# Performance work log

Measured on AMD Instinct MI355X. Metric: run time of the kernel, lower is better.

## Reference

```python
import jax, jax.numpy as jnp
import numpy as np

N = 128 * 128          # hardcoded in the original forward: x.view(1, 1, 128*128)
SCORE_LIMIT = int(0.5 * N)   # int(score_limit * num_inputs) = 8192
K = 7                  # odd kernel_size, padding = K // 2 = 3


def setup_inputs() -> dict:
    key = jax.random.key(0)
    k1, k2 = jax.random.split(key)
    x = jax.random.normal(k1, (N,), dtype=jnp.float32)
    # Conv1d(1, 1, K, bias=False) weight, flattened to a length-K taps vector
    conv_w = jax.random.normal(k2, (K,), dtype=jnp.float32) * 0.1
    return {"x": x, "conv_w": conv_w}


def reference(x, conv_w):
    # torch Conv1d is cross-correlation with 'same' padding (K odd):
    # y[i] = sum_j w[j] * x[i + j - K//2]. jnp.convolve flips the kernel,
    # so pass conv_w reversed to get cross-correlation.
    y = jnp.convolve(x, conv_w[::-1], mode="same")
    attention_score = jax.nn.sigmoid(y)                     # [N]
    attention_index = jnp.argsort(attention_score)          # ascending, [N]
    keep = attention_index[:SCORE_LIMIT]                    # lowest-score indices kept (as in source)
    simple_score = attention_score[keep] + 1.0              # [SCORE_LIMIT]
    # zeros everywhere, scatter rescaled values at kept indices
    new_x = jnp.zeros_like(x).at[keep].set(x[keep] * simple_score)
    return new_x, attention_score
```

## Files before the change

### kernel.cpp

```cpp
#include <hip/hip_runtime.h>
#include <math.h>

#define N 16384
#define LIMIT 8192
#define NT 1024
#define EPT 16

__global__ __launch_bounds__(1024) void fused_kernel(const float* __restrict__ x,
                                                     const float* __restrict__ w,
                                                     float* __restrict__ out) {
    __shared__ unsigned int hist[2048];
    __shared__ unsigned int partial[256];
    __shared__ unsigned long long prefix_sh;
    __shared__ unsigned int r_sh;

    const int tid = threadIdx.x;
    const int base = tid * EPT;

    float wv[7];
#pragma unroll
    for (int t = 0; t < 7; ++t) wv[t] = w[t];

    float win[EPT + 6];
    const float4* xv = (const float4*)(x + base);
#pragma unroll
    for (int q = 0; q < 4; ++q) {
        float4 v = xv[q];
        win[3 + 4*q + 0] = v.x; win[3 + 4*q + 1] = v.y;
        win[3 + 4*q + 2] = v.z; win[3 + 4*q + 3] = v.w;
    }
#pragma unroll
    for (int t = 0; t < 3; ++t) {
        int jl = base - 3 + t;
        win[t] = (jl >= 0) ? x[jl] : 0.f;
        int jr = base + EPT + t;
        win[EPT + 3 + t] = (jr < N) ? x[jr] : 0.f;
    }

    float s[EPT];
#pragma unroll
    for (int k = 0; k < EPT; ++k) {
        float acc = 0.f;
#pragma unroll
        for (int t = 0; t < 7; ++t)
            acc = __fadd_rn(acc, __fmul_rn(win[k + t], wv[t]));
        s[k] = 1.f / (1.f + expf(-acc));
    }

    float4* so = (float4*)(out + N + base);
#pragma unroll
    for (int q = 0; q < 4; ++q)
        so[q] = make_float4(s[4*q], s[4*q+1], s[4*q+2], s[4*q+3]);

    if (tid == 0) { prefix_sh = 0ULL; r_sh = LIMIT - 1; }

    for (int pass = 0; pass < 4; ++pass) {
        const int shift = 33 - 11 * pass;
        hist[tid] = 0u; hist[tid + 1024] = 0u;
        __syncthreads();
        const unsigned long long prefix = prefix_sh;
        const unsigned int r = r_sh;
#pragma unroll
        for (int k = 0; k < EPT; ++k) {
            unsigned long long key = ((unsigned long long)__float_as_uint(s[k]) << 14)
                                     | (unsigned int)(base + k);
            if ((key >> (shift + 11)) == prefix)
                atomicAdd(&hist[(unsigned int)(key >> shift) & 2047u], 1u);
        }
        __syncthreads();
        if (tid < 256) {
            unsigned int p = 0;
#pragma unroll
            for (int k = 0; k < 8; ++k) p += hist[tid * 8 + k];
            partial[tid] = p;
        }
        __syncthreads();
        if (tid < 64) {
            unsigned int p0 = partial[4*tid+0], p1 = partial[4*tid+1],
                         p2 = partial[4*tid+2], p3 = partial[4*tid+3];
            const unsigned int g = p0 + p1 + p2 + p3;
            unsigned int incl = g;
#pragma unroll
            for (int d = 1; d < 64; d <<= 1) {
                unsigned int up = __shfl_up(incl, d, 64);
                if (tid >= d) incl += up;
            }
            unsigned long long ball = __ballot(incl > r);
            int L = __ffsll((unsigned long long)ball) - 1;
            if (tid == L) {
                unsigned int cum = incl - g;
                unsigned int pp[4] = {p0, p1, p2, p3};
                int grp = -1;
#pragma unroll
                for (int k2 = 0; k2 < 4; ++k2) {
                    if (grp < 0) {
                        if (cum + pp[k2] > r) grp = 4*L + k2;
                        else cum += pp[k2];
                    }
                }
                unsigned int c[8];
#pragma unroll
                for (int k2 = 0; k2 < 8; ++k2) c[k2] = hist[grp*8 + k2];
                int b = -1;
#pragma unroll
                for (int k2 = 0; k2 < 8; ++k2) {
                    if (b < 0) {
                        if (cum + c[k2] > r) b = grp*8 + k2;
                        else cum += c[k2];
                    }
                }
                r_sh = r - cum;
                prefix_sh = (prefix << 11) | (unsigned long long)b;
            }
        }
        __syncthreads();
    }
    const unsigned long long T = prefix_sh;

    float4* no = (float4*)(out + base);
#pragma unroll
    for (int q = 0; q < 4; ++q) {
        float4 v;
        float* vp = &v.x;
#pragma unroll
        for (int e = 0; e < 4; ++e) {
            int k = 4*q + e;
            unsigned long long key = ((unsigned long long)__float_as_uint(s[k]) << 14)
                                     | (unsigned int)(base + k);
            vp[e] = (key <= T) ? __fmul_rn(win[3 + k], __fadd_rn(s[k], 1.0f)) : 0.f;
        }
        no[q] = v;
    }
}

extern "C" void kernel_launch(void* const* d_in, const int* in_sizes, int n_in,
                              void* d_out, int out_size, void* d_ws, size_t ws_size,
                              hipStream_t stream) {
    const float* x = (const float*)d_in[0];
    const float* w = (const float*)d_in[1];
    float* out = (float*)d_out;
    fused_kernel<<<1, NT, 0, stream>>>(x, w, out);
}
```

Baseline: 70.51 us.

## Split radix select across 16 cooperative blocks with compacted candidate keys

Moves the work from a single 1024-thread block to 16 cooperative blocks, one element per thread. A first 10-bit histogram pass is reduced across blocks in global memory, separated by grid syncs. Only keys that fall in the selected bucket are compacted into a workspace buffer, and the remaining radix passes run on those candidates alone. This is meant to remove the serial per-thread loop over 16 elements and the four full histogram passes in one block. It adds two grid-wide syncs, global atomics and workspace traffic, and every block redundantly repeats the candidate select.

```diff
diff --git a/kernel.cpp b/kernel.cpp
--- a/kernel.cpp
+++ b/kernel.cpp
@@ -1,136 +1,185 @@
 #include <hip/hip_runtime.h>
+#include <hip/hip_cooperative_groups.h>
 #include <math.h>
+
+namespace cg = cooperative_groups;
 
 #define N 16384
 #define LIMIT 8192
 #define NT 1024
-#define EPT 16
+#define G 16
 
-__global__ __launch_bounds__(1024) void fused_kernel(const float* __restrict__ x,
-                                                     const float* __restrict__ w,
-                                                     float* __restrict__ out) {
-    __shared__ unsigned int hist[2048];
-    __shared__ unsigned int partial[256];
+
+template <int W, int WIDTH>
+__device__ __forceinline__ void scan_select(unsigned int* tot,
+                                            unsigned int* partial,
+                                            unsigned long long* prefix_sh,
+                                            unsigned int* r_sh) {
+    const int tid = threadIdx.x;
+    const unsigned int r = *r_sh;
+    if (tid < 256) {
+        unsigned int p = 0;
+#pragma unroll
+        for (int q = 0; q < W / 4; ++q) {
+            uint4 v = ((const uint4*)tot)[tid * (W / 4) + q];
+            p += v.x + v.y + v.z + v.w;
+        }
+        partial[tid] = p;
+    }
+    __syncthreads();
+    if (tid < 64) {
+        unsigned int p0 = partial[4*tid+0], p1 = partial[4*tid+1],
+                     p2 = partial[4*tid+2], p3 = partial[4*tid+3];
+        const unsigned int g4 = p0 + p1 + p2 + p3;
+        unsigned int incl = g4;
+#pragma unroll
+        for (int d = 1; d < 64; d <<= 1) {
+            unsigned int up = __shfl_up(incl, d, 64);
+            if (tid >= d) incl += up;
+        }
+        unsigned long long ball = __ballot(incl > r);
+        int L = __ffsll((long long)ball) - 1;
+        if (tid == L) {
+            unsigned int cum = incl - g4;
+            unsigned int pp[4] = {p0, p1, p2, p3};
+            int grp = -1;
+#pragma unroll
+            for (int k = 0; k < 4; ++k)
+                if (grp < 0) { if (cum + pp[k] > r) grp = 4*L + k; else cum += pp[k]; }
+            unsigned int c[W];
+#pragma unroll
+            for (int q = 0; q < W / 4; ++q) {
+                uint4 v = ((const uint4*)tot)[grp * (W / 4) + q];
+                c[4*q+0] = v.x; c[4*q+1] = v.y; c[4*q+2] = v.z; c[4*q+3] = v.w;
+            }
+            int b = -1;
+#pragma unroll
+            for (int k = 0; k < W; ++k)
+                if (b < 0) { if (cum + c[k] > r) b = grp * W + k; else cum += c[k]; }
+            *r_sh = r - cum;
+            *prefix_sh = (*prefix_sh << WIDTH) | (unsigned long long)b;
+        }
+    }
+    __syncthreads();
+}
+
+__global__ __launch_bounds__(NT)
+void fused_kernel(const float* __restrict__ x, const float* __restrict__ w,
+                  float* __restrict__ out, unsigned int* __restrict__ ws) {
+    __shared__ __attribute__((aligned(16))) float lds_x[NT + 6];
+    __shared__ __attribute__((aligned(16))) unsigned int hist[4096];
+    __shared__ __attribute__((aligned(16))) unsigned int partial[256];
     __shared__ unsigned long long prefix_sh;
     __shared__ unsigned int r_sh;
 
     const int tid = threadIdx.x;
-    const int base = tid * EPT;
+    const int blk = blockIdx.x;
+    const int base = blk * NT;
+    const int i = base + tid;
+
+    unsigned int* gcnt = ws;
+    unsigned long long* keys = (unsigned long long*)(ws + 16);
+    unsigned int* ghist = ws + 16 + 2 * 16384;
+
+    if (blk == 0 && tid == 0) *gcnt = 0u;
 
     float wv[7];
 #pragma unroll
     for (int t = 0; t < 7; ++t) wv[t] = w[t];
 
-    float win[EPT + 6];
-    const float4* xv = (const float4*)(x + base);
+    lds_x[3 + tid] = x[i];
+    if (tid < 3) {
+        int jl = base - 3 + tid;
+        lds_x[tid] = (jl >= 0) ? x[jl] : 0.f;
+        int jr = base + NT + tid;
+        lds_x[NT + 3 + tid] = (jr < N) ? x[jr] : 0.f;
+    }
+    hist[tid] = 0u;
+    if (tid == 0) { prefix_sh = 0ULL; r_sh = LIMIT - 1; }
+    __syncthreads();
+
+    float acc = 0.f;
 #pragma unroll
-    for (int q = 0; q < 4; ++q) {
-        float4 v = xv[q];
-        win[3 + 4*q + 0] = v.x; win[3 + 4*q + 1] = v.y;
-        win[3 + 4*q + 2] = v.z; win[3 + 4*q + 3] = v.w;
+    for (int t = 0; t < 7; ++t)
+        acc = __fadd_rn(acc, __fmul_rn(lds_x[tid + t], wv[t]));
+    const float s = 1.f / (1.f + expf(-acc));
+    const float xi = lds_x[3 + tid];
+    out[N + i] = s;
+
+    const unsigned long long key =
+        ((unsigned long long)__float_as_uint(s) << 14) | (unsigned int)i;
+
+    atomicAdd(&hist[(unsigned int)(key >> 34)], 1u);
+    __syncthreads();
+    ghist[blk * NT + tid] = hist[tid];
+
+    __threadfence();
+    cg::this_grid().sync();
+
+    unsigned int tsum = 0;
+#pragma unroll
+    for (int b = 0; b < G; ++b) tsum += ghist[b * NT + tid];
+    hist[tid] = tsum;
+    __syncthreads();
+    scan_select<4, 10>(hist, partial, &prefix_sh, &r_sh);
+    const unsigned int b0 = (unsigned int)prefix_sh;
+    const unsigned int r0 = r_sh;
+
+    const bool cand = ((unsigned int)(key >> 34) == b0);
+    const unsigned long long m = __ballot(cand);
+    unsigned int wbase = 0;
+    if ((tid & 63) == 0 && m) wbase = atomicAdd(gcnt, (unsigned int)__popcll(m));
+    wbase = __shfl(wbase, 0, 64);
+    if (cand) {
+        unsigned int pos = wbase +
+            (unsigned int)__popcll(m & ((1ULL << (tid & 63)) - 1ULL));
+        keys[pos] = key;
     }
-#pragma unroll
-    for (int t = 0; t < 3; ++t) {
-        int jl = base - 3 + t;
-        win[t] = (jl >= 0) ? x[jl] : 0.f;
-        int jr = base + EPT + t;
-        win[EPT + 3 + t] = (jr < N) ? x[jr] : 0.f;
+    if (tid == 0) { prefix_sh = 0ULL; r_sh = r0; }
+    __threadfence();
+    cg::this_grid().sync();
+
+    const unsigned int C = __hip_atomic_load(gcnt, __ATOMIC_RELAXED,
+                                             __HIP_MEMORY_SCOPE_AGENT);
+
+    hist[tid] = 0; hist[tid+1024] = 0; hist[tid+2048] = 0; hist[tid+3072] = 0;
+    __syncthreads();
+    for (int j = tid; j < (int)C; j += NT) {
+        unsigned long long k34 = keys[j] & ((1ULL << 34) - 1ULL);
+        atomicAdd(&hist[(unsigned int)(k34 >> 22)], 1u);
     }
+    __syncthreads();
+    scan_select<16, 12>(hist, partial, &prefix_sh, &r_sh);
 
-    float s[EPT];
-#pragma unroll
-    for (int k = 0; k < EPT; ++k) {
-        float acc = 0.f;
-#pragma unroll
-        for (int t = 0; t < 7; ++t)
-            acc = __fadd_rn(acc, __fmul_rn(win[k + t], wv[t]));
-        s[k] = 1.f / (1.f + expf(-acc));
+    hist[tid] = 0; hist[tid+1024] = 0;
+    __syncthreads();
+    {
+        const unsigned long long pref = prefix_sh;
+        for (int j = tid; j < (int)C; j += NT) {
+            unsigned long long k34 = keys[j] & ((1ULL << 34) - 1ULL);
+            if ((k34 >> 22) == pref)
+                atomicAdd(&hist[(unsigned int)(k34 >> 11) & 2047u], 1u);
+        }
     }
+    __syncthreads();
+    scan_select<8, 11>(hist, partial, &prefix_sh, &r_sh);
 
-    float4* so = (float4*)(out + N + base);
-#pragma unroll
-    for (int q = 0; q < 4; ++q)
-        so[q] = make_float4(s[4*q], s[4*q+1], s[4*q+2], s[4*q+3]);
+    hist[tid] = 0; hist[tid+1024] = 0;
+    __syncthreads();
+    {
+        const unsigned long long pref = prefix_sh;
+        for (int j = tid; j < (int)C; j += NT) {
+            unsigned long long k34 = keys[j] & ((1ULL << 34) - 1ULL);
+            if ((k34 >> 11) == pref)
+                atomicAdd(&hist[(unsigned int)k34 & 2047u], 1u);
+        }
+    }
+    __syncthreads();
+    scan_select<8, 11>(hist, partial, &prefix_sh, &r_sh);
 
-    if (tid == 0) { prefix_sh = 0ULL; r_sh = LIMIT - 1; }
+    const unsigned long long T = ((unsigned long long)b0 << 34) | prefix_sh;
 
-    for (int pass = 0; pass < 4; ++pass) {
-        const int shift = 33 - 11 * pass;
-        hist[tid] = 0u; hist[tid + 1024] = 0u;
-        __syncthreads();
-        const unsigned long long prefix = prefix_sh;
-        const unsigned int r = r_sh;
-#pragma unroll
-        for (int k = 0; k < EPT; ++k) {
-            unsigned long long key = ((unsigned long long)__float_as_uint(s[k]) << 14)
-                                     | (unsigned int)(base + k);
-            if ((key >> (shift + 11)) == prefix)
-                atomicAdd(&hist[(unsigned int)(key >> shift) & 2047u], 1u);
-        }
-        __syncthreads();
-        if (tid < 256) {
-            unsigned int p = 0;
-#pragma unroll
-            for (int k = 0; k < 8; ++k) p += hist[tid * 8 + k];
-            partial[tid] = p;
-        }
-        __syncthreads();
-        if (tid < 64) {
-            unsigned int p0 = partial[4*tid+0], p1 = partial[4*tid+1],
-                         p2 = partial[4*tid+2], p3 = partial[4*tid+3];
-            const unsigned int g = p0 + p1 + p2 + p3;
-            unsigned int incl = g;
-#pragma unroll
-            for (int d = 1; d < 64; d <<= 1) {
-                unsigned int up = __shfl_up(incl, d, 64);
-                if (tid >= d) incl += up;
-            }
-            unsigned long long ball = __ballot(incl > r);
-            int L = __ffsll((unsigned long long)ball) - 1;
-            if (tid == L) {
-                unsigned int cum = incl - g;
-                unsigned int pp[4] = {p0, p1, p2, p3};
-                int grp = -1;
-#pragma unroll
-                for (int k2 = 0; k2 < 4; ++k2) {
-                    if (grp < 0) {
-                        if (cum + pp[k2] > r) grp = 4*L + k2;
-                        else cum += pp[k2];
-                    }
-                }
-                unsigned int c[8];
-#pragma unroll
-                for (int k2 = 0; k2 < 8; ++k2) c[k2] = hist[grp*8 + k2];
-                int b = -1;
-#pragma unroll
-                for (int k2 = 0; k2 < 8; ++k2) {
-                    if (b < 0) {
-                        if (cum + c[k2] > r) b = grp*8 + k2;
-                        else cum += c[k2];
-                    }
-                }
-                r_sh = r - cum;
-                prefix_sh = (prefix << 11) | (unsigned long long)b;
-            }
-        }
-        __syncthreads();
-    }
-    const unsigned long long T = prefix_sh;
-
-    float4* no = (float4*)(out + base);
-#pragma unroll
-    for (int q = 0; q < 4; ++q) {
-        float4 v;
-        float* vp = &v.x;
-#pragma unroll
-        for (int e = 0; e < 4; ++e) {
-            int k = 4*q + e;
-            unsigned long long key = ((unsigned long long)__float_as_uint(s[k]) << 14)
-                                     | (unsigned int)(base + k);
-            vp[e] = (key <= T) ? __fmul_rn(win[3 + k], __fadd_rn(s[k], 1.0f)) : 0.f;
-        }
-        no[q] = v;
-    }
+    out[i] = (key <= T) ? __fmul_rn(xi, __fadd_rn(s, 1.0f)) : 0.f;
 }
 
 extern "C" void kernel_launch(void* const* d_in, const int* in_sizes, int n_in,
@@ -139,5 +188,8 @@
     const float* x = (const float*)d_in[0];
     const float* w = (const float*)d_in[1];
     float* out = (float*)d_out;
-    fused_kernel<<<1, NT, 0, stream>>>(x, w, out);
+    unsigned int* ws = (unsigned int*)d_ws;
+    void* args[] = { (void*)&x, (void*)&w, (void*)&out, (void*)&ws };
+    hipLaunchCooperativeKernel((void*)fused_kernel, dim3(G), dim3(NT),
+                               args, 0, stream);
 }
```

Measured after the change: 105.1 us. +49.1%, slower.
